# Performance work log

Measured on AMD Instinct MI355X. Metric: run time of the kernel, lower is better.

The kernel has to match this reference:

```python
import jax, jax.numpy as jnp
import numpy as np

D_MODEL = 16
D_STATE = 16
D_CONV = 4
EXPAND = 2
D_INNER = EXPAND * D_MODEL  # 32
DT_RANK = 1                 # ceil(d_model / 16)
H_MLP = 2 * D_MODEL         # MLP hidden = input_dim * 2
EPS = 1e-6
B, L = 16, 8192


def setup_inputs() -> dict:
    key = jax.random.key(0)
    ks = jax.random.split(key, 20)
    g = lambda i, shape, s: jax.random.normal(ks[i], shape, jnp.float32) * s
    # S4D-real init for A_log, as in mamba_ssm
    A_log = jnp.log(jnp.broadcast_to(jnp.arange(1, D_STATE + 1, dtype=jnp.float32), (D_INNER, D_STATE)))
    return {
        "x": jax.random.normal(ks[0], (B, L, D_MODEL), jnp.float32),
        "rms1_w": jnp.ones((D_MODEL,), jnp.float32),
        "in_proj_w": g(1, (D_MODEL, 2 * D_INNER), 0.25),
        "conv_w": g(2, (D_INNER, D_CONV), 0.3),
        "conv_b": g(3, (D_INNER,), 0.05),
        "x_proj_w": g(4, (D_INNER, DT_RANK + 2 * D_STATE), 0.2),
        "dt_proj_w": g(5, (DT_RANK, D_INNER), 0.5),
        "dt_proj_b": g(6, (D_INNER,), 0.1),
        "A_log": A_log,
        "D_skip": jnp.ones((D_INNER,), jnp.float32),
        "out_proj_w": g(7, (D_INNER, D_MODEL), 0.2),
        "rms2_w": jnp.ones((D_MODEL,), jnp.float32),
        "fc1_w": g(8, (D_MODEL, H_MLP), 0.25),
        "fc1_b": g(9, (H_MLP,), 0.05),
        "fc2_w": g(10, (H_MLP, H_MLP), 0.2),
        "fc2_b": g(11, (H_MLP,), 0.05),
        "fc3_w": g(12, (H_MLP, D_MODEL), 0.2),
        "fc3_b": g(13, (D_MODEL,), 0.05),
    }


def _rmsnorm(h, w):
    v = jnp.mean(h.astype(jnp.float32) ** 2, axis=-1, keepdims=True)
    return w * (h * jax.lax.rsqrt(v + EPS))


def _mamba(x0, in_proj_w, conv_w, conv_b, x_proj_w, dt_proj_w, dt_proj_b, A_log, D_skip, out_proj_w):
    b, l, _ = x0.shape
    xz = x0 @ in_proj_w                      # [B,L,2*Di]
    xm, z = jnp.split(xz, 2, axis=-1)        # each [B,L,Di]
    # causal depthwise conv1d (kernel D_CONV), padding d_conv-1, truncated to L
    xp = jnp.pad(xm, ((0, 0), (D_CONV - 1, 0), (0, 0)))
    xc = conv_b + sum(conv_w[:, k] * xp[:, k:k + l, :] for k in range(D_CONV))
    xc = jax.nn.silu(xc)
    # input-dependent dt, B, C
    proj = xc @ x_proj_w                     # [B,L,dt_rank+2*Ds]
    dt, Bm, Cm = jnp.split(proj, [DT_RANK, DT_RANK + D_STATE], axis=-1)
    dt = jax.nn.softplus(dt @ dt_proj_w + dt_proj_b)   # [B,L,Di]
    A = -jnp.exp(A_log)                      # [Di,Ds]
    deltaA = jnp.exp(dt[..., None] * A)                             # [B,L,Di,Ds]
    deltaBx = dt[..., None] * Bm[:, :, None, :] * xc[..., None]     # [B,L,Di,Ds]
    # sequential selective scan over time (time-major for lax.scan)
    def step(h, inputs):
        dA, dBx, C = inputs                  # [B,Di,Ds],[B,Di,Ds],[B,Ds]
        h = dA * h + dBx
        y = jnp.einsum('bds,bs->bd', h, C)
        return h, y
    h0 = jnp.zeros((b, D_INNER, D_STATE), xc.dtype)
    xs = (deltaA.transpose(1, 0, 2, 3), deltaBx.transpose(1, 0, 2, 3), Cm.transpose(1, 0, 2))
    _, ys = jax.lax.scan(step, h0, xs)       # [L,B,Di]
    y = ys.transpose(1, 0, 2) + D_skip * xc  # [B,L,Di]
    y = y * jax.nn.silu(z)
    return y @ out_proj_w                    # [B,L,Dm]


def reference(x, rms1_w, in_proj_w, conv_w, conv_b, x_proj_w, dt_proj_w, dt_proj_b,
              A_log, D_skip, out_proj_w, rms2_w, fc1_w, fc1_b, fc2_w, fc2_b, fc3_w, fc3_b):
    x0 = _rmsnorm(x, rms1_w)
    x1 = _mamba(x0, in_proj_w, conv_w, conv_b, x_proj_w, dt_proj_w, dt_proj_b, A_log, D_skip, out_proj_w)
    x = x1 + x
    x2 = _rmsnorm(x, rms2_w)
    h = jax.nn.relu(x2 @ fc1_w + fc1_b)
    h = jax.nn.relu(h @ fc2_w + fc2_b)
    x3 = h @ fc3_w + fc3_b
    return x + x3
```

## Files before the change

### kernel.cpp

```cpp
#include <hip/hip_runtime.h>

#define LSEQ 8192
#define NBAT 16
#define DMOD 16
#define DINN 32
#define DSTA 16
#define CL   32
#define NCH  (LSEQ / CL)
#define NCHT (NBAT * NCH)
#define NROWS (NBAT * LSEQ)
#define SUMN ((size_t)NCHT * 512)
#define NSEG 8
#define SEGC (NCH / NSEG)
#define RECU 800
#define LOG2E 1.44269504f

typedef __attribute__((ext_vector_type(8))) short bf16x8;
typedef __attribute__((ext_vector_type(4))) float f32x4;

__device__ __forceinline__ float fsilu(float v) { return v / (1.f + __expf(-v)); }
__device__ __forceinline__ float fsoftplus(float v) {
  return v > 20.f ? v : __logf(1.f + __expf(v));
}
__device__ __forceinline__ unsigned packbf(float a, float b) {
  unsigned r;
  asm("v_cvt_pk_bf16_f32 %0, %1, %2" : "=v"(r) : "v"(a), "v"(b));
  return r;
}
__device__ __forceinline__ short f2bf(float f) {
  return (short)(packbf(f, f) & 0xffffu);
}
__device__ __forceinline__ float bf2f(short s) {
  union { unsigned u; float f; } v;
  v.u = ((unsigned)(unsigned short)s) << 16;
  return v.f;
}
__device__ __forceinline__ float bflo(unsigned u) {
  union { unsigned a; float f; } v; v.a = u << 16; return v.f;
}
__device__ __forceinline__ float bfhi(unsigned u) {
  union { unsigned a; float f; } v; v.a = u & 0xffff0000u; return v.f;
}

__device__ __forceinline__ void load_x_row(const float* __restrict__ x, long r,
                                           float* __restrict__ xr) {
  const float4* xp = reinterpret_cast<const float4*>(x + r * DMOD);
  float4 v0 = xp[0], v1 = xp[1], v2 = xp[2], v3 = xp[3];
  xr[0] = v0.x; xr[1] = v0.y; xr[2] = v0.z; xr[3] = v0.w;
  xr[4] = v1.x; xr[5] = v1.y; xr[6] = v1.z; xr[7] = v1.w;
  xr[8] = v2.x; xr[9] = v2.y; xr[10] = v2.z; xr[11] = v2.w;
  xr[12] = v3.x; xr[13] = v3.y; xr[14] = v3.z; xr[15] = v3.w;
}

__device__ __forceinline__ f32x4 mm(bf16x8 a, bf16x8 b, f32x4 c) {
  return __builtin_amdgcn_mfma_f32_16x16x32_bf16(a, b, c, 0, 0, 0);
}
__device__ __forceinline__ bf16x8 bfrag(const float* __restrict__ W, int ldw,
                                        int coloff, int col, int kg, int kreal) {
  bf16x8 b = {0, 0, 0, 0, 0, 0, 0, 0};
#pragma unroll
  for (int e = 0; e < 8; e++) {
    int k = kg * 8 + e;
    if (k < kreal) b[e] = f2bf(W[k * ldw + coloff + col]);
  }
  return b;
}

__global__ __launch_bounds__(256) void k_prep(
    const float* __restrict__ x, const float* __restrict__ rms1w,
    const float* __restrict__ ipw, const float* __restrict__ cw,
    const float* __restrict__ cb, const float* __restrict__ xpw,
    const float* __restrict__ dtw, const float* __restrict__ dtb,
    const float* __restrict__ A_log, const float* __restrict__ Dskip,
    unsigned* __restrict__ rec, float* __restrict__ Pb,
    float* __restrict__ Hb) {
  __shared__ short xmv[67][36];
  __shared__ short x0b[64][40];
  __shared__ short xcb[64][40];
  int t = threadIdx.x;
  int lane = t & 63, wid = t >> 6;
  int col = lane & 15, kg = lane >> 4;
  long row0 = (long)blockIdx.x * 64;
  int l0 = (int)(row0 & (LSEQ - 1));
  const f32x4 zero4 = {0.f, 0.f, 0.f, 0.f};

  bf16x8 Bip0 = bfrag(ipw, 64, 0, col, kg, 16);
  bf16x8 Bip1 = bfrag(ipw, 64, 16, col, kg, 16);
  bf16x8 Bdt, Bb, Bc;
#pragma unroll
  for (int e = 0; e < 8; e++) {
    int k = kg * 8 + e;
    Bdt[e] = (col == 0) ? f2bf(xpw[k * 33]) : (short)0;
    Bb[e] = f2bf(xpw[k * 33 + 1 + col]);
    Bc[e] = f2bf(xpw[k * 33 + 17 + col]);
  }

  if (t < 128) {
    int row = t >> 1, hf = t & 1;
    const float4* xp =
        reinterpret_cast<const float4*>(x + (row0 + row) * DMOD + hf * 8);
    float4 v0 = xp[0], v1 = xp[1];
    float xr[8] = {v0.x, v0.y, v0.z, v0.w, v1.x, v1.y, v1.z, v1.w};
    float ss = 0.f;
#pragma unroll
    for (int i = 0; i < 8; i++) ss += xr[i] * xr[i];
    ss += __shfl_xor(ss, 1);
    float inv1 = rsqrtf(ss * (1.f / 16.f) + 1e-6f);
    unsigned u[4];
#pragma unroll
    for (int i = 0; i < 4; i++)
      u[i] = packbf(xr[2 * i] * inv1 * rms1w[hf * 8 + 2 * i],
                    xr[2 * i + 1] * inv1 * rms1w[hf * 8 + 2 * i + 1]);
    *reinterpret_cast<uint4*>(&x0b[row][hf * 8]) =
        make_uint4(u[0], u[1], u[2], u[3]);
  } else if (t < 224) {
    int h = (t - 128) >> 5, k = (t - 128) & 31;
    short v = 0;
    if (l0 != 0) {
      float xr[16];
      load_x_row(x, row0 - 3 + h, xr);
      float ss = 0.f;
#pragma unroll
      for (int i = 0; i < 16; i++) ss += xr[i] * xr[i];
      float inv1 = rsqrtf(ss * (1.f / 16.f) + 1e-6f);
      float acc = 0.f;
#pragma unroll
      for (int i = 0; i < 16; i++)
        acc = fmaf(xr[i] * inv1 * rms1w[i], ipw[i * 64 + k], acc);
      v = f2bf(acc);
    }
    xmv[h][k] = v;
  }
  __syncthreads();

  {
    int arow = wid * 16 + col;
    bf16x8 a = {0, 0, 0, 0, 0, 0, 0, 0};
    if (kg < 2) a = *reinterpret_cast<const bf16x8*>(&x0b[arow][kg * 8]);
    f32x4 m0 = mm(a, Bip0, zero4);
    f32x4 m1 = mm(a, Bip1, zero4);
    int orow = 3 + wid * 16 + kg * 4;
#pragma unroll
    for (int reg = 0; reg < 4; reg++) {
      unsigned p = packbf(m0[reg], m1[reg]);
      xmv[orow + reg][col] = (short)(p & 0xffffu);
      xmv[orow + reg][col + 16] = (short)(p >> 16);
    }
  }
  __syncthreads();

  {
    int row = t >> 2, q = t & 3;
    unsigned u[4];
#pragma unroll
    for (int dp = 0; dp < 4; dp++) {
      int d = q * 8 + dp * 2;
      float ce = cb[d], co = cb[d + 1];
#pragma unroll
      for (int k = 0; k < 4; k++) {
        unsigned xu = *reinterpret_cast<const unsigned*>(&xmv[row + k][d]);
        ce = fmaf(cw[d * 4 + k], bflo(xu), ce);
        co = fmaf(cw[(d + 1) * 4 + k], bfhi(xu), co);
      }
      u[dp] = packbf(fsilu(ce), fsilu(co));
    }
    *reinterpret_cast<uint4*>(&xcb[row][q * 8]) =
        make_uint4(u[0], u[1], u[2], u[3]);
  }
  __syncthreads();

  {
    int arow = wid * 16 + col;
    bf16x8 a2 = *reinterpret_cast<const bf16x8*>(&xcb[arow][kg * 8]);
    f32x4 pd = mm(a2, Bdt, zero4);
    f32x4 pb = mm(a2, Bb, zero4);
    f32x4 pc = mm(a2, Bc, zero4);
    int orow = wid * 16 + kg * 4;
#pragma unroll
    for (int reg = 0; reg < 4; reg++) {
      unsigned p = packbf(pb[reg], pc[reg]);
      xmv[orow + reg][col] = (short)(p & 0xffffu);
      xmv[orow + reg][16 + col] = (short)(p >> 16);
      if (col == 0) xmv[orow + reg][32] = f2bf(pd[reg]);
    }
  }
  __syncthreads();

  {
    int row = t >> 2, q = t & 3;
    float p0 = bf2f(xmv[row][32]);
    unsigned u[4];
#pragma unroll
    for (int dp = 0; dp < 4; dp++) {
      int d = q * 8 + dp * 2;
      u[dp] = packbf(fsoftplus(fmaf(p0, dtw[d], dtb[d])),
                     fsoftplus(fmaf(p0, dtw[d + 1], dtb[d + 1])));
    }
    *reinterpret_cast<uint4*>(&x0b[row][q * 8]) =
        make_uint4(u[0], u[1], u[2], u[3]);
  }
  __syncthreads();

  {
    int ch = t >> 7, b128 = t & 127;
    int d = b128 >> 2, s4 = (b128 & 3) << 2;
    float Ad0 = -__expf(A_log[d * 16 + s4 + 0]) * LOG2E;
    float Ad1 = -__expf(A_log[d * 16 + s4 + 1]) * LOG2E;
    float Ad2 = -__expf(A_log[d * 16 + s4 + 2]) * LOG2E;
    float Ad3 = -__expf(A_log[d * 16 + s4 + 3]) * LOG2E;
    float dskd = Dskip[d];
    bool w0 = (t & 3) == 0;
    float H0 = 0.f, H1 = 0.f, H2 = 0.f, H3 = 0.f, cum = 0.f;
#pragma unroll 4
    for (int li = 0; li < CL; li++) {
      int row = ch * CL + li;
      float dt = bf2f(x0b[row][d]);
      float xcv = bf2f(xcb[row][d]);
      float dx = dt * xcv;
      cum += dt;
      uint2 bu = *reinterpret_cast<const uint2*>(&xmv[row][s4]);
      uint2 cu = *reinterpret_cast<const uint2*>(&xmv[row][16 + s4]);
      float a;
      a = __builtin_amdgcn_exp2f(dt * Ad0); H0 = fmaf(a, H0, dx * bflo(bu.x));
      a = __builtin_amdgcn_exp2f(dt * Ad1); H1 = fmaf(a, H1, dx * bfhi(bu.x));
      a = __builtin_amdgcn_exp2f(dt * Ad2); H2 = fmaf(a, H2, dx * bflo(bu.y));
      a = __builtin_amdgcn_exp2f(dt * Ad3); H3 = fmaf(a, H3, dx * bfhi(bu.y));
      float py = bflo(cu.x) * H0;
      py = fmaf(bfhi(cu.x), H1, py);
      py = fmaf(bflo(cu.y), H2, py);
      py = fmaf(bfhi(cu.y), H3, py);
      py += __shfl_xor(py, 1);
      py += __shfl_xor(py, 2);
      if (w0) xcb[row][d] = f2bf(fmaf(dskd, xcv, py));
    }
    size_t sb_ = (size_t)(blockIdx.x * 2 + ch) * 512 + (size_t)(d * 16 + s4);
    *reinterpret_cast<float4*>(Pb + sb_) = make_float4(
        __builtin_amdgcn_exp2f(cum * Ad0), __builtin_amdgcn_exp2f(cum * Ad1),
        __builtin_amdgcn_exp2f(cum * Ad2), __builtin_amdgcn_exp2f(cum * Ad3));
    *reinterpret_cast<float4*>(Hb + sb_) = make_float4(H0, H1, H2, H3);
  }
  __syncthreads();

  {
    unsigned* rb0 = rec + (size_t)(blockIdx.x * 2) * RECU;
#pragma unroll
    for (int i = 0; i < 7; i++) {
      int idx = i * 256 + t;
      if (idx < 1600) {
        int ch = idx / 800;
        int rem = idx - ch * 800;
        int c = rem >> 5, l = rem & 31;
        int row = ch * 32 + l;
        unsigned val;
        if (c < 16)
          val = *reinterpret_cast<const unsigned*>(&xcb[row][2 * c]);
        else if (c < 24)
          val = *reinterpret_cast<const unsigned*>(&xmv[row][16 + 2 * (c - 16)]);
        else
          val = (unsigned)(unsigned short)xmv[row][32];
        rb0[ch * RECU + rem] = val;
      }
    }
  }
}

__global__ __launch_bounds__(256) void k_seg(float* __restrict__ Pb,
                                             float* __restrict__ Hb,
                                             float* __restrict__ segP,
                                             float* __restrict__ segH) {
  int g = blockIdx.x * 256 + threadIdx.x;
  int b = g >> 12;
  int rem = g & 4095;
  int seg = rem >> 9, st = rem & 511;
  size_t o = ((size_t)(b * NCH + seg * SEGC)) * 512 + st;
  float h = 0.f, p = 1.f;
#pragma unroll 4
  for (int c = 0; c < SEGC; c++) {
    float P = Pb[o], H = Hb[o];
    Pb[o] = p;
    Hb[o] = h;
    h = fmaf(P, h, H);
    p *= P;
    o += 512;
  }
  size_t so = (size_t)(b * NSEG + seg) * 512 + st;
  segP[so] = p;
  segH[so] = h;
}

__global__ __launch_bounds__(256) void k_carry(const float* __restrict__ segP,
                                               const float* __restrict__ segH,
                                               float* __restrict__ carry) {
  int g = blockIdx.x * 256 + threadIdx.x;
  int b = g >> 9, st = g & 511;
  float h = 0.f;
#pragma unroll
  for (int s = 0; s < NSEG; s++) {
    size_t so = (size_t)(b * NSEG + s) * 512 + st;
    carry[so] = h;
    h = fmaf(segP[so], h, segH[so]);
  }
}

__global__ __launch_bounds__(256) void k_mlp(
    const unsigned* __restrict__ rec, const float* __restrict__ x,
    const float* __restrict__ A_log, const float* __restrict__ Pb,
    const float* __restrict__ Hb, const float* __restrict__ carry,
    const float* __restrict__ dtw, const float* __restrict__ dtb,
    const float* __restrict__ rms1w, const float* __restrict__ ipw,
    const float* __restrict__ opw, const float* __restrict__ rms2w,
    const float* __restrict__ f1w, const float* __restrict__ f1b,
    const float* __restrict__ f2w, const float* __restrict__ f2b,
    const float* __restrict__ f3w, const float* __restrict__ f3b,
    float* __restrict__ out) {
  __shared__ float h0L[8 * 516];
  __shared__ float Ads[512];
  __shared__ short sbx[256][24];
  __shared__ short sby[256][40];
  int t = threadIdx.x, bc = blockIdx.x;
  long row0 = (long)bc * 256;

  Ads[t] = -__expf(A_log[t]) * LOG2E;
  Ads[256 + t] = -__expf(A_log[256 + t]) * LOG2E;
#pragma unroll
  for (int i = 0; i < 16; i++) {
    int idx = i * 256 + t;
    int chl = idx >> 9, st = idx & 511;
    int gc = bc * 8 + chl;
    size_t o = (size_t)gc * 512 + st;
    int b = gc >> 8, seg = (gc >> 5) & 7;
    h0L[chl * 516 + st] =
        fmaf(Pb[o], carry[(size_t)(b * NSEG + seg) * 512 + st], Hb[o]);
  }
  {
    float xr[16];
    load_x_row(x, row0 + t, xr);
    float ss = 0.f;
#pragma unroll
    for (int i = 0; i < 16; i++) ss += xr[i] * xr[i];
    float inv1 = rsqrtf(ss * (1.f / 16.f) + 1e-6f);
    unsigned u[8];
#pragma unroll
    for (int i = 0; i < 8; i++)
      u[i] = packbf(xr[2 * i] * inv1 * rms1w[2 * i],
                    xr[2 * i + 1] * inv1 * rms1w[2 * i + 1]);
    *reinterpret_cast<uint4*>(&sbx[t][0]) = make_uint4(u[0], u[1], u[2], u[3]);
    *reinterpret_cast<uint4*>(&sbx[t][8]) = make_uint4(u[4], u[5], u[6], u[7]);
  }
  __syncthreads();

  {
    int ch = t >> 5, l = t & 31;
    const unsigned* rb = rec + (size_t)(bc * 8 + ch) * RECU;
    float Cv[16];
#pragma unroll
    for (int c = 0; c < 8; c++) {
      unsigned u = rb[(16 + c) * 32 + l];
      Cv[2 * c] = bflo(u);
      Cv[2 * c + 1] = bfhi(u);
    }
    float p0 = bflo(rb[24 * 32 + l]);
    int lm = t & 31;
    float cum[32];
#pragma unroll
    for (int d = 0; d < 32; d++) {
      float dtv = fsoftplus(fmaf(p0, dtw[d], dtb[d]));
#pragma unroll
      for (int dl = 1; dl < 32; dl <<= 1) {
        float u_ = __shfl_up(dtv, dl, 32);
        if (lm >= dl) dtv += u_;
      }
      cum[d] = dtv;
    }
    const float* h0c = &h0L[ch * 516];
#pragma unroll
    for (int dp = 0; dp < 16; dp++) {
      unsigned yu = rb[dp * 32 + l];
      float acc0 = bflo(yu), acc1 = bfhi(yu);
      float cd0 = cum[2 * dp], cd1 = cum[2 * dp + 1];
      int dof0 = dp * 32, dof1 = dp * 32 + 16;
#pragma unroll
      for (int s = 0; s < 16; s++) {
        float e0 = __builtin_amdgcn_exp2f(Ads[dof0 + s] * cd0);
        float e1 = __builtin_amdgcn_exp2f(Ads[dof1 + s] * cd1);
        acc0 = fmaf(e0 * Cv[s], h0c[dof0 + s], acc0);
        acc1 = fmaf(e1 * Cv[s], h0c[dof1 + s], acc1);
      }
      *reinterpret_cast<unsigned*>(&sby[t][2 * dp]) = packbf(acc0, acc1);
    }
  }
  __syncthreads();

  {
    int lane = t & 63, w = t >> 6;
    int col = lane & 15, kg = lane >> 4;
    bf16x8 Bz0 = bfrag(ipw + 32, 64, 0, col, kg, 16);
    bf16x8 Bz1 = bfrag(ipw + 32, 64, 16, col, kg, 16);
    bf16x8 Bop = bfrag(opw, 16, 0, col, kg, 32);
    bf16x8 Bf1_0 = bfrag(f1w, 32, 0, col, kg, 16);
    bf16x8 Bf1_1 = bfrag(f1w, 32, 16, col, kg, 16);
    bf16x8 Bf2_0 = bfrag(f2w, 32, 0, col, kg, 32);
    bf16x8 Bf2_1 = bfrag(f2w, 32, 16, col, kg, 32);
    bf16x8 Bf3 = bfrag(f3w, 16, 0, col, kg, 32);
    float b1_0 = f1b[col], b1_1 = f1b[16 + col];
    float b2_0 = f2b[col], b2_1 = f2b[16 + col];
    float b3c = f3b[col], rw2 = rms2w[col];
    const f32x4 zero4 = {0.f, 0.f, 0.f, 0.f};
#pragma unroll 1
    for (int rt = 0; rt < 4; rt++) {
      int tile0 = w * 64 + rt * 16;
      bf16x8 ax0 = {0, 0, 0, 0, 0, 0, 0, 0};
      if (kg < 2) ax0 = *reinterpret_cast<const bf16x8*>(&sbx[tile0 + col][kg * 8]);
      f32x4 zf0 = mm(ax0, Bz0, zero4);
      f32x4 zf1 = mm(ax0, Bz1, zero4);
#pragma unroll
      for (int reg = 0; reg < 4; reg++) {
        int lrow = tile0 + kg * 4 + reg;
        unsigned yu = *reinterpret_cast<const unsigned*>(&sby[lrow][0]) ;
        float y0 = bf2f(sby[lrow][col]);
        float y1 = bf2f(sby[lrow][16 + col]);
        (void)yu;
        unsigned p = packbf(y0 * fsilu(zf0[reg]), y1 * fsilu(zf1[reg]));
        sby[lrow][col] = (short)(p & 0xffffu);
        sby[lrow][16 + col] = (short)(p >> 16);
      }
      bf16x8 ayo = *reinterpret_cast<const bf16x8*>(&sby[tile0 + col][kg * 8]);
      f32x4 x1f = mm(ayo, Bop, zero4);
      float xres[4];
#pragma unroll
      for (int reg = 0; reg < 4; reg++) {
        long grow = row0 + tile0 + kg * 4 + reg;
        xres[reg] = x1f[reg] + x[grow * 16 + col];
      }
#pragma unroll
      for (int reg = 0; reg < 4; reg++) {
        float ss = xres[reg] * xres[reg];
        ss += __shfl_xor(ss, 1);
        ss += __shfl_xor(ss, 2);
        ss += __shfl_xor(ss, 4);
        ss += __shfl_xor(ss, 8);
        float inv2 = rsqrtf(ss * (1.f / 16.f) + 1e-6f);
        sby[tile0 + kg * 4 + reg][col] = f2bf(xres[reg] * inv2 * rw2);
      }
      bf16x8 ax2 = {0, 0, 0, 0, 0, 0, 0, 0};
      if (kg < 2) ax2 = *reinterpret_cast<const bf16x8*>(&sby[tile0 + col][kg * 8]);
      f32x4 h1f0 = mm(ax2, Bf1_0, zero4);
      f32x4 h1f1 = mm(ax2, Bf1_1, zero4);
#pragma unroll
      for (int reg = 0; reg < 4; reg++) {
        int lrow = tile0 + kg * 4 + reg;
        unsigned p = packbf(fmaxf(h1f0[reg] + b1_0, 0.f),
                            fmaxf(h1f1[reg] + b1_1, 0.f));
        sby[lrow][col] = (short)(p & 0xffffu);
        sby[lrow][16 + col] = (short)(p >> 16);
      }
      bf16x8 ah1 = *reinterpret_cast<const bf16x8*>(&sby[tile0 + col][kg * 8]);
      f32x4 h2f0 = mm(ah1, Bf2_0, zero4);
      f32x4 h2f1 = mm(ah1, Bf2_1, zero4);
#pragma unroll
      for (int reg = 0; reg < 4; reg++) {
        int lrow = tile0 + kg * 4 + reg;
        unsigned p = packbf(fmaxf(h2f0[reg] + b2_0, 0.f),
                            fmaxf(h2f1[reg] + b2_1, 0.f));
        sby[lrow][col] = (short)(p & 0xffffu);
        sby[lrow][16 + col] = (short)(p >> 16);
      }
      bf16x8 ah2 = *reinterpret_cast<const bf16x8*>(&sby[tile0 + col][kg * 8]);
      f32x4 x3f = mm(ah2, Bf3, zero4);
#pragma unroll
      for (int reg = 0; reg < 4; reg++) {
        long grow = row0 + tile0 + kg * 4 + reg;
        out[grow * 16 + col] = xres[reg] + x3f[reg] + b3c;
      }
    }
  }
}

extern "C" void kernel_launch(void* const* d_in, const int* in_sizes, int n_in,
                              void* d_out, int out_size, void* d_ws,
                              size_t ws_size, hipStream_t stream) {
  const float* x = (const float*)d_in[0];
  const float* rms1w = (const float*)d_in[1];
  const float* ipw = (const float*)d_in[2];
  const float* cw = (const float*)d_in[3];
  const float* cb = (const float*)d_in[4];
  const float* xpw = (const float*)d_in[5];
  const float* dtw = (const float*)d_in[6];
  const float* dtb = (const float*)d_in[7];
  const float* A_log = (const float*)d_in[8];
  const float* Dskip = (const float*)d_in[9];
  const float* opw = (const float*)d_in[10];
  const float* rms2w = (const float*)d_in[11];
  const float* f1w = (const float*)d_in[12];
  const float* f1b = (const float*)d_in[13];
  const float* f2w = (const float*)d_in[14];
  const float* f2b = (const float*)d_in[15];
  const float* f3w = (const float*)d_in[16];
  const float* f3b = (const float*)d_in[17];
  float* out = (float*)d_out;

  unsigned* rec = (unsigned*)d_ws;
  float* Pb = (float*)(rec + (size_t)NCHT * RECU);
  float* Hb = Pb + SUMN;
  float* segP = Hb + SUMN;
  float* segH = segP + NBAT * NSEG * 512;
  float* carry = segH + NBAT * NSEG * 512;

  hipLaunchKernelGGL(k_prep, dim3(NROWS / 64), dim3(256), 0, stream, x, rms1w,
                     ipw, cw, cb, xpw, dtw, dtb, A_log, Dskip, rec, Pb, Hb);
  hipLaunchKernelGGL(k_seg, dim3(256), dim3(256), 0, stream, Pb, Hb, segP,
                     segH);
  hipLaunchKernelGGL(k_carry, dim3(32), dim3(256), 0, stream, segP, segH,
                     carry);
  hipLaunchKernelGGL(k_mlp, dim3(NROWS / 256), dim3(256), 0, stream, rec, x,
                     A_log, Pb, Hb, carry, dtw, dtb, rms1w, ipw, opw, rms2w,
                     f1w, f1b, f2w, f2b, f3w, f3b, out);
}
```

Before: 88.48 us.

## Halve rows per block in k_mlp and split per-row work across thread pairs

The final fused kernel now handles 128 rows per 256-thread block instead of 256. Two threads share each row: they split the RMSNorm load with a shuffle reduction, and in the inter-chunk correction each thread covers half of the inner channels. The cumsum is computed on the fly per channel pair, which removes the 32-element cum register array and should lower register pressure. The cost is twice as many blocks, each recomputing Ads, and only 2 MFMA tiles per wave, so per-block overhead is amortized over less work.

```diff
diff --git a/kernel.cpp b/kernel.cpp
--- a/kernel.cpp
+++ b/kernel.cpp
@@ -313,45 +313,49 @@
     const float* __restrict__ f2w, const float* __restrict__ f2b,
     const float* __restrict__ f3w, const float* __restrict__ f3b,
     float* __restrict__ out) {
-  __shared__ float h0L[8 * 516];
+  __shared__ float h0L[4 * 516];
   __shared__ float Ads[512];
-  __shared__ short sbx[256][24];
-  __shared__ short sby[256][40];
+  __shared__ short sbx[128][24];
+  __shared__ short sby[128][40];
   int t = threadIdx.x, bc = blockIdx.x;
-  long row0 = (long)bc * 256;
+  long row0 = (long)bc * 128;
 
   Ads[t] = -__expf(A_log[t]) * LOG2E;
   Ads[256 + t] = -__expf(A_log[256 + t]) * LOG2E;
 #pragma unroll
-  for (int i = 0; i < 16; i++) {
+  for (int i = 0; i < 8; i++) {
     int idx = i * 256 + t;
     int chl = idx >> 9, st = idx & 511;
-    int gc = bc * 8 + chl;
+    int gc = bc * 4 + chl;
     size_t o = (size_t)gc * 512 + st;
     int b = gc >> 8, seg = (gc >> 5) & 7;
     h0L[chl * 516 + st] =
         fmaf(Pb[o], carry[(size_t)(b * NSEG + seg) * 512 + st], Hb[o]);
   }
   {
-    float xr[16];
-    load_x_row(x, row0 + t, xr);
+    int row = t >> 1, hf = t & 1;
+    const float4* xp =
+        reinterpret_cast<const float4*>(x + (row0 + row) * DMOD + hf * 8);
+    float4 v0 = xp[0], v1 = xp[1];
+    float xr[8] = {v0.x, v0.y, v0.z, v0.w, v1.x, v1.y, v1.z, v1.w};
     float ss = 0.f;
 #pragma unroll
-    for (int i = 0; i < 16; i++) ss += xr[i] * xr[i];
+    for (int i = 0; i < 8; i++) ss += xr[i] * xr[i];
+    ss += __shfl_xor(ss, 1);
     float inv1 = rsqrtf(ss * (1.f / 16.f) + 1e-6f);
-    unsigned u[8];
-#pragma unroll
-    for (int i = 0; i < 8; i++)
-      u[i] = packbf(xr[2 * i] * inv1 * rms1w[2 * i],
-                    xr[2 * i + 1] * inv1 * rms1w[2 * i + 1]);
-    *reinterpret_cast<uint4*>(&sbx[t][0]) = make_uint4(u[0], u[1], u[2], u[3]);
-    *reinterpret_cast<uint4*>(&sbx[t][8]) = make_uint4(u[4], u[5], u[6], u[7]);
-  }
-  __syncthreads();
-
-  {
-    int ch = t >> 5, l = t & 31;
-    const unsigned* rb = rec + (size_t)(bc * 8 + ch) * RECU;
+    unsigned u[4];
+#pragma unroll
+    for (int i = 0; i < 4; i++)
+      u[i] = packbf(xr[2 * i] * inv1 * rms1w[hf * 8 + 2 * i],
+                    xr[2 * i + 1] * inv1 * rms1w[hf * 8 + 2 * i + 1]);
+    *reinterpret_cast<uint4*>(&sbx[t >> 1][hf * 8]) =
+        make_uint4(u[0], u[1], u[2], u[3]);
+  }
+  __syncthreads();
+
+  {
+    int ch = t >> 6, half = (t >> 5) & 1, l = t & 31;
+    const unsigned* rb = rec + (size_t)(bc * 4 + ch) * RECU;
     float Cv[16];
 #pragma unroll
     for (int c = 0; c < 8; c++) {
@@ -360,25 +364,23 @@
       Cv[2 * c + 1] = bfhi(u);
     }
     float p0 = bflo(rb[24 * 32 + l]);
-    int lm = t & 31;
-    float cum[32];
-#pragma unroll
-    for (int d = 0; d < 32; d++) {
-      float dtv = fsoftplus(fmaf(p0, dtw[d], dtb[d]));
+    const float* h0c = &h0L[ch * 516];
+    int row = ch * 32 + l;
+#pragma unroll
+    for (int cc = 0; cc < 8; cc++) {
+      int c = half * 8 + cc;
+      int d0 = 2 * c, d1 = 2 * c + 1;
+      float cd0 = fsoftplus(fmaf(p0, dtw[d0], dtb[d0]));
+      float cd1 = fsoftplus(fmaf(p0, dtw[d1], dtb[d1]));
 #pragma unroll
       for (int dl = 1; dl < 32; dl <<= 1) {
-        float u_ = __shfl_up(dtv, dl, 32);
-        if (lm >= dl) dtv += u_;
-      }
-      cum[d] = dtv;
-    }
-    const float* h0c = &h0L[ch * 516];
-#pragma unroll
-    for (int dp = 0; dp < 16; dp++) {
-      unsigned yu = rb[dp * 32 + l];
+        float u0 = __shfl_up(cd0, dl, 32);
+        float u1 = __shfl_up(cd1, dl, 32);
+        if (l >= dl) { cd0 += u0; cd1 += u1; }
+      }
+      unsigned yu = rb[c * 32 + l];
       float acc0 = bflo(yu), acc1 = bfhi(yu);
-      float cd0 = cum[2 * dp], cd1 = cum[2 * dp + 1];
-      int dof0 = dp * 32, dof1 = dp * 32 + 16;
+      int dof0 = d0 * 16, dof1 = d1 * 16;
 #pragma unroll
       for (int s = 0; s < 16; s++) {
         float e0 = __builtin_amdgcn_exp2f(Ads[dof0 + s] * cd0);
@@ -386,7 +388,7 @@
         acc0 = fmaf(e0 * Cv[s], h0c[dof0 + s], acc0);
         acc1 = fmaf(e1 * Cv[s], h0c[dof1 + s], acc1);
       }
-      *reinterpret_cast<unsigned*>(&sby[t][2 * dp]) = packbf(acc0, acc1);
+      *reinterpret_cast<unsigned*>(&sby[row][2 * c]) = packbf(acc0, acc1);
     }
   }
   __syncthreads();
@@ -407,8 +409,8 @@
     float b3c = f3b[col], rw2 = rms2w[col];
     const f32x4 zero4 = {0.f, 0.f, 0.f, 0.f};
 #pragma unroll 1
-    for (int rt = 0; rt < 4; rt++) {
-      int tile0 = w * 64 + rt * 16;
+    for (int rt = 0; rt < 2; rt++) {
+      int tile0 = w * 32 + rt * 16;
       bf16x8 ax0 = {0, 0, 0, 0, 0, 0, 0, 0};
       if (kg < 2) ax0 = *reinterpret_cast<const bf16x8*>(&sbx[tile0 + col][kg * 8]);
       f32x4 zf0 = mm(ax0, Bz0, zero4);
@@ -416,10 +418,8 @@
 #pragma unroll
       for (int reg = 0; reg < 4; reg++) {
         int lrow = tile0 + kg * 4 + reg;
-        unsigned yu = *reinterpret_cast<const unsigned*>(&sby[lrow][0]) ;
         float y0 = bf2f(sby[lrow][col]);
         float y1 = bf2f(sby[lrow][16 + col]);
-        (void)yu;
         unsigned p = packbf(y0 * fsilu(zf0[reg]), y1 * fsilu(zf1[reg]));
         sby[lrow][col] = (short)(p & 0xffffu);
         sby[lrow][16 + col] = (short)(p >> 16);
@@ -512,7 +512,7 @@
                      segH);
   hipLaunchKernelGGL(k_carry, dim3(32), dim3(256), 0, stream, segP, segH,
                      carry);
-  hipLaunchKernelGGL(k_mlp, dim3(NROWS / 256), dim3(256), 0, stream, rec, x,
+  hipLaunchKernelGGL(k_mlp, dim3(NROWS / 128), dim3(256), 0, stream, rec, x,
                      A_log, Pb, Hb, carry, dtw, dtb, rms1w, ipw, opw, rms2w,
                      f1w, f1b, f2w, f2b, f3w, f3b, out);
 }
```

New measurement: 84.67 us. 1.04x faster.
